# Kernel tuning notes

Measured on AMD Instinct MI355X. Metric: run time of the kernel, lower is better.

The kernel has to match this reference:

```python
import jax, jax.numpy as jnp
import numpy as np
import math

DIM = 1280
NUM_HEADS = 16
HEAD_DIM = DIM // NUM_HEADS  # 80
SEQ = 3072


def setup_inputs() -> dict:
    key = jax.random.key(0)
    ks = jax.random.split(key, 6)
    hidden_states = jax.random.normal(ks[0], (SEQ, DIM), dtype=jnp.float32)
    cu_seqlens = jnp.array([0, 768, 1536, 2304, 3072], dtype=jnp.int32)
    # rotary angles for half the head dim, as produced by the vision rotary embedding
    rotary_pos_emb = jax.random.uniform(ks[1], (SEQ, HEAD_DIM // 2), dtype=jnp.float32) * 10.0
    qkv_w = jax.random.normal(ks[2], (3 * DIM, DIM), dtype=jnp.float32) * (1.0 / math.sqrt(DIM))
    qkv_b = jax.random.normal(ks[3], (3 * DIM,), dtype=jnp.float32) * 0.02
    proj_w = jax.random.normal(ks[4], (DIM, DIM), dtype=jnp.float32) * (1.0 / math.sqrt(DIM))
    proj_b = jax.random.normal(ks[5], (DIM,), dtype=jnp.float32) * 0.02
    return {"hidden_states": hidden_states, "cu_seqlens": cu_seqlens,
            "rotary_pos_emb": rotary_pos_emb, "qkv_w": qkv_w, "qkv_b": qkv_b,
            "proj_w": proj_w, "proj_b": proj_b}


def _rotate_half(x):
    half = x.shape[-1] // 2
    return jnp.concatenate([-x[..., half:], x[..., :half]], axis=-1)


def _apply_rotary(t, rotary_pos_emb):
    # t: [seq, heads, head_dim]; rotary_pos_emb: [seq, head_dim//2]
    emb = jnp.concatenate([rotary_pos_emb, rotary_pos_emb], axis=-1)  # [seq, head_dim]
    cos = jnp.cos(emb)[:, None, :]
    sin = jnp.sin(emb)[:, None, :]
    return t * cos + _rotate_half(t) * sin


def reference(hidden_states, cu_seqlens, rotary_pos_emb, qkv_w, qkv_b, proj_w, proj_b):
    seq = hidden_states.shape[0]
    qkv = hidden_states @ qkv_w.T + qkv_b                       # [seq, 3*dim]
    qkv = qkv.reshape(seq, 3, NUM_HEADS, HEAD_DIM)
    q, k, v = qkv[:, 0], qkv[:, 1], qkv[:, 2]                   # [seq, h, d]
    q = _apply_rotary(q, rotary_pos_emb)
    k = _apply_rotary(k, rotary_pos_emb)

    # block-diagonal mask: token i attends to token j iff same segment
    seg = jnp.searchsorted(cu_seqlens[1:], jnp.arange(seq), side='right')
    same = seg[:, None] == seg[None, :]                         # [seq, seq] bool
    neg = jnp.finfo(q.dtype).min
    add_mask = jnp.where(same, jnp.float32(0), neg).astype(q.dtype)

    scale = 1.0 / math.sqrt(HEAD_DIM)
    scores = jnp.einsum('nhd,mhd->hnm', q, k) * scale           # [h, seq, seq]
    scores = scores + add_mask[None, :, :]
    attn = jax.nn.softmax(scores.astype(jnp.float32), axis=-1).astype(q.dtype)
    out = jnp.einsum('hnm,mhd->nhd', attn, v).reshape(seq, DIM)
    return out @ proj_w.T + proj_b
```

## Files before the change

### kernel.cpp

```cpp
#include <hip/hip_runtime.h>

#define SEQ 3072
#define NH 16
#define HD 80
#define SEGLEN 768

typedef unsigned short u16;
typedef unsigned int u32;
typedef float f32x4 __attribute__((ext_vector_type(4)));
typedef __bf16 bf16x8 __attribute__((ext_vector_type(8)));
typedef short short8 __attribute__((ext_vector_type(8)));
typedef u16 u16x4 __attribute__((ext_vector_type(4)));

#define WAITV(N) asm volatile("s_waitcnt vmcnt(" #N ")" ::: "memory")

__device__ __forceinline__ u16 f2bf(float f) {
  u32 u = __builtin_bit_cast(u32, f);
  u32 r = u + 0x7fffu + ((u >> 16) & 1u);
  return (u16)(r >> 16);
}
__device__ __forceinline__ float bf2f(u16 x) {
  u32 u = ((u32)x) << 16;
  return __builtin_bit_cast(float, u);
}

__device__ __forceinline__ f32x4 mfma16(short8 a, short8 b, f32x4 c) {
  return __builtin_amdgcn_mfma_f32_16x16x32_bf16(
      __builtin_bit_cast(bf16x8, a), __builtin_bit_cast(bf16x8, b), c, 0, 0, 0);
}

__device__ __forceinline__ void gload_lds16(const u16* g, u16* l) {
  __builtin_amdgcn_global_load_lds(
      (const __attribute__((address_space(1))) u32*)(g),
      (__attribute__((address_space(3))) u32*)(l), 16, 0, 0);
}

__global__ __launch_bounds__(256) void cvt3(const float* __restrict__ a, u16* __restrict__ ao, int na,
                                            const float* __restrict__ b, u16* __restrict__ bo, int nb,
                                            const float* __restrict__ c, u16* __restrict__ co, int nc) {
  int i = blockIdx.x * 256 + threadIdx.x;
  const float* src;
  u16* dst;
  int n;
  if (i < na) { src = a; dst = ao; n = i; }
  else if (i < na + nb) { src = b; dst = bo; n = i - na; }
  else if (i < na + nb + nc) { src = c; dst = co; n = i - na - nb; }
  else return;
  f32x4 v = ((const f32x4*)src)[n];
  u16x4 o;
  o[0] = f2bf(v[0]); o[1] = f2bf(v[1]); o[2] = f2bf(v[2]); o[3] = f2bf(v[3]);
  ((u16x4*)dst)[n] = o;
}

__global__ __launch_bounds__(512) void gemm_192(
    const u16* __restrict__ A, const u16* __restrict__ B,
    const float* __restrict__ bias, u16* __restrict__ C,
    int M, int N, int K) {
  __shared__ u16 LB[2 * 28672];
  char* lds = (char*)LB;
  const int tid = threadIdx.x, lane = tid & 63, w = tid >> 6;
  const int wm = w >> 2, wn = w & 3;
  const int lr = lane & 15, lg = lane >> 4;
  const int br = blockIdx.y * 192, bc = blockIdx.x * 256;
  const int NT = K >> 6;

  f32x4 acc[6][4];
#pragma unroll
  for (int m = 0; m < 6; ++m)
#pragma unroll
    for (int n = 0; n < 4; ++n) acc[m][n] = (f32x4){0.f, 0.f, 0.f, 0.f};

  const int chA0 = w * 96 + lane, chA1 = w * 96 + 64 + lane;
  const int chB0 = w * 128 + lane, chB1 = w * 128 + 64 + lane;
  auto srcptr = [&](const u16* Mx, int base, int ch, int Kd) {
    int row = ch >> 2, sl = ch & 3;
    return Mx + (size_t)(base + row) * Kd + (((sl - (row >> 1)) & 3) << 3);
  };
  const u16* sA0 = srcptr(A, br, chA0, K);
  const u16* sA1 = srcptr(A, br, chA1 < 768 ? chA1 : chA0, K);
  const u16* sB0 = srcptr(B, bc, chB0, K);
  const u16* sB1 = srcptr(B, bc, chB1, K);

  auto stgA = [&](int kcol, int buf, int half) {
    char* hb = lds + buf * 57344 + half * 12288;
    gload_lds16(sA0 + kcol, (u16*)(hb + chA0 * 16));
    if (lane < 32) gload_lds16(sA1 + kcol, (u16*)(hb + chA1 * 16));
  };
  auto stgB = [&](int kcol, int buf, int half) {
    char* hb = lds + buf * 57344 + 24576 + half * 16384;
    gload_lds16(sB0 + kcol, (u16*)(hb + chB0 * 16));
    gload_lds16(sB1 + kcol, (u16*)(hb + chB1 * 16));
  };

  int aoff[6], boff[4];
#pragma unroll
  for (int m = 0; m < 6; ++m) {
    int row = wm * 96 + m * 16 + lr;
    aoff[m] = row * 64 + ((lg + (row >> 1)) & 3) * 16;
  }
#pragma unroll
  for (int n = 0; n < 4; ++n) {
    int row = wn * 64 + n * 16 + lr;
    boff[n] = row * 64 + ((lg + (row >> 1)) & 3) * 16;
  }

  stgA(0, 0, 0); stgB(0, 0, 0);
  stgA(32, 0, 1); stgB(32, 0, 1);
  WAITV(4);
  __builtin_amdgcn_s_barrier();

  for (int t = 0; t < NT; ++t) {
    const int p = t & 1;
    const char* bufb = lds + p * 57344;
#pragma unroll
    for (int q = 0; q < 2; ++q) {
      const char* Ah = bufb + q * 12288;
      const char* Bh = bufb + 24576 + q * 16384;
      short8 af[6], bf[4];
#pragma unroll
      for (int m = 0; m < 6; ++m) af[m] = *(const short8*)(Ah + aoff[m]);
#pragma unroll
      for (int n = 0; n < 4; ++n) bf[n] = *(const short8*)(Bh + boff[n]);
      if (t + 1 < NT) {
        stgA((t + 1) * 64 + q * 32, p ^ 1, q);
        stgB((t + 1) * 64 + q * 32, p ^ 1, q);
      }
      __builtin_amdgcn_s_setprio(1);
#pragma unroll
      for (int m = 0; m < 6; ++m)
#pragma unroll
        for (int n = 0; n < 4; ++n) acc[m][n] = mfma16(af[m], bf[n], acc[m][n]);
      __builtin_amdgcn_s_setprio(0);
      if (t + 1 < NT) {
        WAITV(4);
        __builtin_amdgcn_s_barrier();
      } else if (q == 0) {
        WAITV(0);
        __builtin_amdgcn_s_barrier();
      }
    }
  }

#pragma unroll
  for (int n = 0; n < 4; ++n) {
    int col = bc + wn * 64 + n * 16 + lr;
    float bv = bias[col];
#pragma unroll
    for (int m = 0; m < 6; ++m) {
      int rowb = br + wm * 96 + m * 16 + lg * 4;
#pragma unroll
      for (int r = 0; r < 4; ++r)
        C[(size_t)(rowb + r) * N + col] = f2bf(acc[m][n][r] + bv);
    }
  }
}

template <int OUT_BF16, int WM, int WN>
__global__ __launch_bounds__(256) void gemm_p3(
    const u16* __restrict__ A, const u16* __restrict__ B,
    const float* __restrict__ bias, void* __restrict__ Cv,
    int M, int N, int K) {
  constexpr int BM = 32 * WM, BN = 32 * WN;
  constexpr int ROWS = BM + BN;
  constexpr int L = ROWS / 64;
  static_assert(L == 3, "tuned for L=3");
  __shared__ u16 LB[3][ROWS * 32];
  const int tid = threadIdx.x, lane = tid & 63, w = tid >> 6;
  const int wr = (w >> 1) * (WM * 16), wc = (w & 1) * (WN * 16);
  const int lr = lane & 15, lg = lane >> 4;
  const int gy = gridDim.y;
  const int fc = blockIdx.x * gy + blockIdx.y;
  const int cpx = (gridDim.x * gy) >> 3;
  const int f = (fc & 7) * cpx + (fc >> 3);
  const int bx = f / gy, by = f % gy;
  const int br = by * BM, bc = bx * BN;
  const int NT = K >> 5;

  f32x4 acc[WM][WN];
#pragma unroll
  for (int m = 0; m < WM; ++m)
#pragma unroll
    for (int n = 0; n < WN; ++n) acc[m][n] = (f32x4){0.f, 0.f, 0.f, 0.f};

  const u16* sp[L];
#pragma unroll
  for (int c = 0; c < L; ++c) {
    int ch = c * 256 + tid;
    int row = ch >> 2, sl = ch & 3;
    int scol = ((sl - (row >> 1)) & 3) << 3;
    sp[c] = (row < BM ? A + (br + row) * (size_t)K
                      : B + (bc + row - BM) * (size_t)K) + scol;
  }
  auto stage = [&](int t, int buf) {
#pragma unroll
    for (int c = 0; c < L; ++c)
      gload_lds16(sp[c] + t * 32, &LB[buf][(c * 256 + tid) * 8]);
  };

  int aoff[WM], boff[WN];
#pragma unroll
  for (int m = 0; m < WM; ++m) {
    int row = wr + m * 16 + lr;
    aoff[m] = row * 64 + ((lg + (row >> 1)) & 3) * 16;
  }
#pragma unroll
  for (int n = 0; n < WN; ++n) {
    int row = BM + wc + n * 16 + lr;
    boff[n] = row * 64 + ((lg + (row >> 1)) & 3) * 16;
  }

  auto step = [&](int t, int buf, bool issue, int wn) {
    if (issue) stage(t + 2, (t + 2) % 3);
    const char* base = (const char*)&LB[buf][0];
    short8 af[WM], bf[WN];
#pragma unroll
    for (int m = 0; m < WM; ++m) af[m] = *(const short8*)(base + aoff[m]);
#pragma unroll
    for (int n = 0; n < WN; ++n) bf[n] = *(const short8*)(base + boff[n]);
#pragma unroll
    for (int m = 0; m < WM; ++m)
#pragma unroll
      for (int n = 0; n < WN; ++n) acc[m][n] = mfma16(af[m], bf[n], acc[m][n]);
    if (wn == 3) WAITV(3);
    else if (wn == 0) WAITV(0);
    if (wn >= 0) __builtin_amdgcn_s_barrier();
  };

  stage(0, 0);
  stage(1, 1);
  WAITV(3);
  __builtin_amdgcn_s_barrier();

  int t = 0;
  for (; t + 3 <= NT - 2; t += 3) {
    step(t + 0, 0, true, 3);
    step(t + 1, 1, true, 3);
    step(t + 2, 2, true, 3);
  }
  step(NT - 4, 0, true, 3);
  step(NT - 3, 1, true, 3);
  step(NT - 2, 2, false, 0);
  step(NT - 1, 0, false, -1);

#pragma unroll
  for (int n = 0; n < WN; ++n) {
    int col = bc + wc + n * 16 + lr;
    float bv = bias[col];
#pragma unroll
    for (int m = 0; m < WM; ++m) {
      int rowb = br + wr + m * 16 + lg * 4;
#pragma unroll
      for (int r = 0; r < 4; ++r) {
        float v = acc[m][n][r] + bv;
        if (OUT_BF16)
          ((u16*)Cv)[(rowb + r) * N + col] = f2bf(v);
        else
          ((float*)Cv)[(rowb + r) * N + col] = v;
      }
    }
  }
}

__global__ __launch_bounds__(256) void prep_kern(
    const u16* __restrict__ qkvb, const float* __restrict__ rpe,
    u16* __restrict__ qb, u16* __restrict__ kb, u16* __restrict__ vt) {
  const int bid = blockIdx.x, tid = threadIdx.x;
  if (bid < 3072) {
    const float QSCL = 0.16129841769519493f;
    const u16* row = qkvb + bid * 3840;
#pragma unroll
    for (int it = 0; it < 5; ++it) {
      int idx = it * 256 + tid;
      int d = idx % 80;
      float e = rpe[bid * 40 + (d % 40)];
      float s, c;
      sincosf(e, &s, &c);
      float qv = bf2f(row[idx]);
      float qo = (d < 40) ? -bf2f(row[idx + 40]) : bf2f(row[idx - 40]);
      float kv = bf2f(row[1280 + idx]);
      float ko = (d < 40) ? -bf2f(row[1280 + idx + 40]) : bf2f(row[1280 + idx - 40]);
      int o = bid * 1280 + idx;
      qb[o] = f2bf((qv * c + qo * s) * QSCL);
      kb[o] = f2bf(kv * c + ko * s);
    }
  } else {
    __shared__ u16 tile[64 * 84];
    const int vb = bid - 3072;
    const int s0 = (vb % 48) * 64, h = vb / 48;
#pragma unroll
    for (int c = 0; c < 20; ++c) {
      int ch = c * 256 + tid;
      int r = ch / 80, d = ch % 80;
      tile[r * 84 + d] = qkvb[(s0 + r) * 3840 + 2560 + h * 80 + d];
    }
    __syncthreads();
#pragma unroll
    for (int c = 0; c < 20; ++c) {
      int ch = c * 256 + tid;
      int d = ch >> 6, r = ch & 63;
      vt[(h * 96 + d) * 3072 + s0 + r] = tile[r * 84 + d];
    }
    if (tid < 64) vt[(h * 96 + 80) * 3072 + s0 + tid] = 0x3F80;
  }
}

__global__ __launch_bounds__(256) void attn_kern(
    const u16* __restrict__ qb, const u16* __restrict__ kb,
    const u16* __restrict__ vt, u16* __restrict__ ob) {
  __shared__ u16 SH[26176];
  char* shb = (char*)SH;
  const int tid = threadIdx.x, lane = tid & 63, w = tid >> 6;
  const int lr = lane & 15, lg = lane >> 4;
  const int xcd = blockIdx.x & 7, t = blockIdx.x >> 3;
  const int qt = t % 12, shhi = t / 12;
  const int sh = xcd + shhi * 8;
  const int seg = sh >> 4, h = sh & 15;
  const int qrow = seg * SEGLEN + qt * 64 + w * 16 + lr;

  short8 qf[3];
#pragma unroll
  for (int kk = 0; kk < 3; ++kk) {
    int d = kk * 32 + lg * 8;
    if (d < 80)
      qf[kk] = *(const short8*)(qb + qrow * 1280 + h * 80 + d);
    else
      qf[kk] = (short8){0, 0, 0, 0, 0, 0, 0, 0};
  }
  f32x4 oa[6];
#pragma unroll
  for (int n = 0; n < 6; ++n) oa[n] = (f32x4){0.f, 0.f, 0.f, 0.f};
  float mrow[4] = {-1e30f, -1e30f, -1e30f, -1e30f};

  const u16* kseg = kb + seg * SEGLEN * 1280 + h * 80;
  const u16* vseg = vt + (h * 96) * 3072 + seg * SEGLEN;

  auto stageK = [&](int buf, int it) {
    const u16* kbase = kseg + it * 64 * 1280;
#pragma unroll
    for (int c = 0; c < 4; ++c) {
      int ch = c * 256 + tid;
      int kv = ch >> 4, sl = ch & 15;
      gload_lds16(kbase + kv * 1280 + ((sl ^ (kv & 7)) << 3),
                  (u16*)(shb + buf * 16384 + ch * 16));
    }
  };
  auto stageV = [&](int it) {
    const u16* vbase = vseg + it * 64;
#pragma unroll
    for (int c = 0; c < 3; ++c) {
      int ch = c * 256 + tid;
      if (ch < 648) {
        int d = ch >> 3, sl = ch & 7;
        gload_lds16(vbase + d * 3072 + ((sl ^ (d & 7)) << 3),
                    (u16*)(shb + 32768 + ch * 16));
      }
    }
  };

  stageK(0, 0);
  stageV(0);
  __syncthreads();
  int cur = 0;
  char* PsW = shb + 43136 + w * 2304;
  const char* Vc = shb + 32768;

  for (int it = 0; it < 12; ++it) {
    if (it > 0) stageV(it);
    if (it < 11) stageK(cur ^ 1, it + 1);
    const char* Kc = shb + cur * 16384;
    f32x4 sf[4];
#pragma unroll
    for (int n = 0; n < 4; ++n) {
      sf[n] = (f32x4){0.f, 0.f, 0.f, 0.f};
#pragma unroll
      for (int kk = 0; kk < 3; ++kk) {
        int row = n * 16 + lr;
        int X = kk * 64 + lg * 16;
        short8 kf = *(const short8*)(Kc + row * 256 + (X ^ ((row & 7) << 4)));
        __builtin_amdgcn_s_setprio(1);
        sf[n] = mfma16(qf[kk], kf, sf[n]);
        __builtin_amdgcn_s_setprio(0);
      }
    }
    float mx[4];
#pragma unroll
    for (int r = 0; r < 4; ++r) {
      float a = fmaxf(fmaxf(sf[0][r], sf[1][r]), fmaxf(sf[2][r], sf[3][r]));
      a = fmaxf(a, __shfl_xor(a, 1, 16));
      a = fmaxf(a, __shfl_xor(a, 2, 16));
      a = fmaxf(a, __shfl_xor(a, 4, 16));
      a = fmaxf(a, __shfl_xor(a, 8, 16));
      mx[r] = a;
    }
    float need = fmaxf(fmaxf(mx[0] - mrow[0], mx[1] - mrow[1]),
                       fmaxf(mx[2] - mrow[2], mx[3] - mrow[3]));
    if (!__all(need <= 8.0f)) {
#pragma unroll
      for (int r = 0; r < 4; ++r) {
        float m = fmaxf(mrow[r], mx[r]);
        float f = exp2f(mrow[r] - m);
        mrow[r] = m;
#pragma unroll
        for (int n = 0; n < 6; ++n) oa[n][r] *= f;
      }
    }
#pragma unroll
    for (int r = 0; r < 4; ++r) {
      float p0 = exp2f(sf[0][r] - mrow[r]), p1 = exp2f(sf[1][r] - mrow[r]);
      float p2 = exp2f(sf[2][r] - mrow[r]), p3 = exp2f(sf[3][r] - mrow[r]);
      int offb = (lg * 4 + r) * 144 + lr * 2;
      *(u16*)(PsW + offb + ((lg ^ 0) << 5)) = f2bf(p0);
      *(u16*)(PsW + offb + ((lg ^ 1) << 5)) = f2bf(p1);
      *(u16*)(PsW + offb + ((lg ^ 2) << 5)) = f2bf(p2);
      *(u16*)(PsW + offb + ((lg ^ 3) << 5)) = f2bf(p3);
    }
    __syncthreads();
#pragma unroll
    for (int kt = 0; kt < 2; ++kt) {
      short8 pf = *(const short8*)(PsW + lr * 144 +
                                   ((((kt << 1) + (lg >> 1)) ^ (lr >> 2)) << 5) +
                                   ((lg & 1) << 4));
#pragma unroll
      for (int n = 0; n < 6; ++n) {
        int dcol = n * 16 + lr;
        int X = kt * 64 + lg * 16;
        short8 vf = *(const short8*)(Vc + dcol * 128 + (X ^ ((dcol & 7) << 4)));
        __builtin_amdgcn_s_setprio(1);
        oa[n] = mfma16(pf, vf, oa[n]);
        __builtin_amdgcn_s_setprio(0);
      }
    }
    __syncthreads();
    cur ^= 1;
  }
#pragma unroll
  for (int r = 0; r < 4; ++r) {
    float lsum = __shfl(oa[5][r], lane & 48, 64);
    float linv = 1.0f / lsum;
    int orow = seg * SEGLEN + qt * 64 + w * 16 + lg * 4 + r;
#pragma unroll
    for (int n = 0; n < 5; ++n)
      ob[orow * 1280 + h * 80 + n * 16 + lr] = f2bf(oa[n][r] * linv);
  }
}

extern "C" void kernel_launch(void* const* d_in, const int* in_sizes, int n_in,
                              void* d_out, int out_size, void* d_ws, size_t ws_size,
                              hipStream_t stream) {
  const float* hs = (const float*)d_in[0];
  const float* rpe = (const float*)d_in[2];
  const float* qkvw = (const float*)d_in[3];
  const float* qkv_b = (const float*)d_in[4];
  const float* pw = (const float*)d_in[5];
  const float* pb = (const float*)d_in[6];
  float* out = (float*)d_out;

  char* ws = (char*)d_ws;
  u16* hsb = (u16*)(ws);
  u16* wqkvb = (u16*)(ws + 7864320);
  u16* wprojb = (u16*)(ws + 17694720);
  u16* qkvb = (u16*)(ws + 20971520);
  u16* vt = (u16*)(ws + 44564480);
  u16* qb = hsb;
  u16* kb = wqkvb;
  u16* aob = qkvb;

  cvt3<<<10240, 256, 0, stream>>>(hs, hsb, 983040, qkvw, wqkvb, 1228800, pw, wprojb, 409600);
  gemm_192<<<dim3(15, 16), 512, 0, stream>>>(hsb, wqkvb, qkv_b, qkvb, 3072, 3840, 1280);
  prep_kern<<<3840, 256, 0, stream>>>(qkvb, rpe, qb, kb, vt);
  attn_kern<<<768, 256, 0, stream>>>(qb, kb, vt, aob);
  gemm_p3<0, 2, 4><<<dim3(10, 48), 256, 0, stream>>>(aob, wprojb, pb, out, 3072, 1280, 1280);
}
```

Measured before the change: 127.0 us.

## Process two query sub-tiles per wave in attention with half the threads

The attention kernel now runs 128 threads per block, and each wave handles 32 query rows as two 16-row MFMA tiles. Each K and V fragment read from LDS is reused for two MFMAs. The aim is to cut LDS read traffic and block-level overhead per query row. In exchange, register pressure roughly doubles for accumulators and Q fragments, each thread issues twice as many staging loads, and fewer waves are available to hide latency.

After: 136.2 us. 1.07x slower.

```diff
diff --git a/kernel.cpp b/kernel.cpp
--- a/kernel.cpp
+++ b/kernel.cpp
@@ -304,7 +304,7 @@
   }
 }
 
-__global__ __launch_bounds__(256) void attn_kern(
+__global__ __launch_bounds__(128) void attn_kern(
     const u16* __restrict__ qb, const u16* __restrict__ kb,
     const u16* __restrict__ vt, u16* __restrict__ ob) {
   __shared__ u16 SH[26176];
@@ -315,21 +315,26 @@
   const int qt = t % 12, shhi = t / 12;
   const int sh = xcd + shhi * 8;
   const int seg = sh >> 4, h = sh & 15;
-  const int qrow = seg * SEGLEN + qt * 64 + w * 16 + lr;
-
-  short8 qf[3];
-#pragma unroll
-  for (int kk = 0; kk < 3; ++kk) {
-    int d = kk * 32 + lg * 8;
-    if (d < 80)
-      qf[kk] = *(const short8*)(qb + qrow * 1280 + h * 80 + d);
-    else
-      qf[kk] = (short8){0, 0, 0, 0, 0, 0, 0, 0};
-  }
-  f32x4 oa[6];
-#pragma unroll
-  for (int n = 0; n < 6; ++n) oa[n] = (f32x4){0.f, 0.f, 0.f, 0.f};
-  float mrow[4] = {-1e30f, -1e30f, -1e30f, -1e30f};
+  const int qbase = seg * SEGLEN + qt * 64 + w * 32;
+
+  short8 qf[2][3];
+#pragma unroll
+  for (int m = 0; m < 2; ++m)
+#pragma unroll
+    for (int kk = 0; kk < 3; ++kk) {
+      int d = kk * 32 + lg * 8;
+      if (d < 80)
+        qf[m][kk] = *(const short8*)(qb + (qbase + m * 16 + lr) * 1280 + h * 80 + d);
+      else
+        qf[m][kk] = (short8){0, 0, 0, 0, 0, 0, 0, 0};
+    }
+  f32x4 oa[2][6];
+#pragma unroll
+  for (int m = 0; m < 2; ++m)
+#pragma unroll
+    for (int n = 0; n < 6; ++n) oa[m][n] = (f32x4){0.f, 0.f, 0.f, 0.f};
+  float mrow[2][4] = {{-1e30f, -1e30f, -1e30f, -1e30f},
+                      {-1e30f, -1e30f, -1e30f, -1e30f}};
 
   const u16* kseg = kb + seg * SEGLEN * 1280 + h * 80;
   const u16* vseg = vt + (h * 96) * 3072 + seg * SEGLEN;
@@ -337,8 +342,8 @@
   auto stageK = [&](int buf, int it) {
     const u16* kbase = kseg + it * 64 * 1280;
 #pragma unroll
-    for (int c = 0; c < 4; ++c) {
-      int ch = c * 256 + tid;
+    for (int c = 0; c < 8; ++c) {
+      int ch = c * 128 + tid;
       int kv = ch >> 4, sl = ch & 15;
       gload_lds16(kbase + kv * 1280 + ((sl ^ (kv & 7)) << 3),
                   (u16*)(shb + buf * 16384 + ch * 16));
@@ -347,8 +352,8 @@
   auto stageV = [&](int it) {
     const u16* vbase = vseg + it * 64;
 #pragma unroll
-    for (int c = 0; c < 3; ++c) {
-      int ch = c * 256 + tid;
+    for (int c = 0; c < 6; ++c) {
+      int ch = c * 128 + tid;
       if (ch < 648) {
         int d = ch >> 3, sl = ch & 7;
         gload_lds16(vbase + d * 3072 + ((sl ^ (d & 7)) << 3),
@@ -361,72 +366,80 @@
   stageV(0);
   __syncthreads();
   int cur = 0;
-  char* PsW = shb + 43136 + w * 2304;
+  char* PsW[2] = {shb + 43136 + (w * 2 + 0) * 2304, shb + 43136 + (w * 2 + 1) * 2304};
   const char* Vc = shb + 32768;
 
   for (int it = 0; it < 12; ++it) {
     if (it > 0) stageV(it);
     if (it < 11) stageK(cur ^ 1, it + 1);
     const char* Kc = shb + cur * 16384;
-    f32x4 sf[4];
+    f32x4 sf[2][4];
+#pragma unroll
+    for (int m = 0; m < 2; ++m)
+#pragma unroll
+      for (int n = 0; n < 4; ++n) sf[m][n] = (f32x4){0.f, 0.f, 0.f, 0.f};
 #pragma unroll
     for (int n = 0; n < 4; ++n) {
-      sf[n] = (f32x4){0.f, 0.f, 0.f, 0.f};
 #pragma unroll
       for (int kk = 0; kk < 3; ++kk) {
         int row = n * 16 + lr;
         int X = kk * 64 + lg * 16;
         short8 kf = *(const short8*)(Kc + row * 256 + (X ^ ((row & 7) << 4)));
         __builtin_amdgcn_s_setprio(1);
-        sf[n] = mfma16(qf[kk], kf, sf[n]);
+        sf[0][n] = mfma16(qf[0][kk], kf, sf[0][n]);
+        sf[1][n] = mfma16(qf[1][kk], kf, sf[1][n]);
         __builtin_amdgcn_s_setprio(0);
       }
     }
-    float mx[4];
-#pragma unroll
-    for (int r = 0; r < 4; ++r) {
-      float a = fmaxf(fmaxf(sf[0][r], sf[1][r]), fmaxf(sf[2][r], sf[3][r]));
-      a = fmaxf(a, __shfl_xor(a, 1, 16));
-      a = fmaxf(a, __shfl_xor(a, 2, 16));
-      a = fmaxf(a, __shfl_xor(a, 4, 16));
-      a = fmaxf(a, __shfl_xor(a, 8, 16));
-      mx[r] = a;
-    }
-    float need = fmaxf(fmaxf(mx[0] - mrow[0], mx[1] - mrow[1]),
-                       fmaxf(mx[2] - mrow[2], mx[3] - mrow[3]));
-    if (!__all(need <= 8.0f)) {
+#pragma unroll
+    for (int m = 0; m < 2; ++m) {
+      float mx[4];
 #pragma unroll
       for (int r = 0; r < 4; ++r) {
-        float m = fmaxf(mrow[r], mx[r]);
-        float f = exp2f(mrow[r] - m);
-        mrow[r] = m;
-#pragma unroll
-        for (int n = 0; n < 6; ++n) oa[n][r] *= f;
-      }
-    }
-#pragma unroll
-    for (int r = 0; r < 4; ++r) {
-      float p0 = exp2f(sf[0][r] - mrow[r]), p1 = exp2f(sf[1][r] - mrow[r]);
-      float p2 = exp2f(sf[2][r] - mrow[r]), p3 = exp2f(sf[3][r] - mrow[r]);
-      int offb = (lg * 4 + r) * 144 + lr * 2;
-      *(u16*)(PsW + offb + ((lg ^ 0) << 5)) = f2bf(p0);
-      *(u16*)(PsW + offb + ((lg ^ 1) << 5)) = f2bf(p1);
-      *(u16*)(PsW + offb + ((lg ^ 2) << 5)) = f2bf(p2);
-      *(u16*)(PsW + offb + ((lg ^ 3) << 5)) = f2bf(p3);
+        float a = fmaxf(fmaxf(sf[m][0][r], sf[m][1][r]), fmaxf(sf[m][2][r], sf[m][3][r]));
+        a = fmaxf(a, __shfl_xor(a, 1, 16));
+        a = fmaxf(a, __shfl_xor(a, 2, 16));
+        a = fmaxf(a, __shfl_xor(a, 4, 16));
+        a = fmaxf(a, __shfl_xor(a, 8, 16));
+        mx[r] = a;
+      }
+      float need = fmaxf(fmaxf(mx[0] - mrow[m][0], mx[1] - mrow[m][1]),
+                         fmaxf(mx[2] - mrow[m][2], mx[3] - mrow[m][3]));
+      if (!__all(need <= 8.0f)) {
+#pragma unroll
+        for (int r = 0; r < 4; ++r) {
+          float mm = fmaxf(mrow[m][r], mx[r]);
+          float f = exp2f(mrow[m][r] - mm);
+          mrow[m][r] = mm;
+#pragma unroll
+          for (int n = 0; n < 6; ++n) oa[m][n][r] *= f;
+        }
+      }
+#pragma unroll
+      for (int r = 0; r < 4; ++r) {
+        float p0 = exp2f(sf[m][0][r] - mrow[m][r]), p1 = exp2f(sf[m][1][r] - mrow[m][r]);
+        float p2 = exp2f(sf[m][2][r] - mrow[m][r]), p3 = exp2f(sf[m][3][r] - mrow[m][r]);
+        int offb = (lg * 4 + r) * 144 + lr * 2;
+        *(u16*)(PsW[m] + offb + ((lg ^ 0) << 5)) = f2bf(p0);
+        *(u16*)(PsW[m] + offb + ((lg ^ 1) << 5)) = f2bf(p1);
+        *(u16*)(PsW[m] + offb + ((lg ^ 2) << 5)) = f2bf(p2);
+        *(u16*)(PsW[m] + offb + ((lg ^ 3) << 5)) = f2bf(p3);
+      }
     }
     __syncthreads();
 #pragma unroll
     for (int kt = 0; kt < 2; ++kt) {
-      short8 pf = *(const short8*)(PsW + lr * 144 +
-                                   ((((kt << 1) + (lg >> 1)) ^ (lr >> 2)) << 5) +
-                                   ((lg & 1) << 4));
+      const int pswz = lr * 144 + ((((kt << 1) + (lg >> 1)) ^ (lr >> 2)) << 5) + ((lg & 1) << 4);
+      short8 pf0 = *(const short8*)(PsW[0] + pswz);
+      short8 pf1 = *(const short8*)(PsW[1] + pswz);
 #pragma unroll
       for (int n = 0; n < 6; ++n) {
         int dcol = n * 16 + lr;
         int X = kt * 64 + lg * 16;
         short8 vf = *(const short8*)(Vc + dcol * 128 + (X ^ ((dcol & 7) << 4)));
         __builtin_amdgcn_s_setprio(1);
-        oa[n] = mfma16(pf, vf, oa[n]);
+        oa[0][n] = mfma16(pf0, vf, oa[0][n]);
+        oa[1][n] = mfma16(pf1, vf, oa[1][n]);
         __builtin_amdgcn_s_setprio(0);
       }
     }
@@ -434,14 +447,16 @@
     cur ^= 1;
   }
 #pragma unroll
-  for (int r = 0; r < 4; ++r) {
-    float lsum = __shfl(oa[5][r], lane & 48, 64);
-    float linv = 1.0f / lsum;
-    int orow = seg * SEGLEN + qt * 64 + w * 16 + lg * 4 + r;
-#pragma unroll
-    for (int n = 0; n < 5; ++n)
-      ob[orow * 1280 + h * 80 + n * 16 + lr] = f2bf(oa[n][r] * linv);
-  }
+  for (int m = 0; m < 2; ++m)
+#pragma unroll
+    for (int r = 0; r < 4; ++r) {
+      float lsum = __shfl(oa[m][5][r], lane & 48, 64);
+      float linv = 1.0f / lsum;
+      int orow = qbase + m * 16 + lg * 4 + r;
+#pragma unroll
+      for (int n = 0; n < 5; ++n)
+        ob[orow * 1280 + h * 80 + n * 16 + lr] = f2bf(oa[m][n][r] * linv);
+    }
 }
 
 extern "C" void kernel_launch(void* const* d_in, const int* in_sizes, int n_in,
@@ -468,6 +483,6 @@
   cvt3<<<10240, 256, 0, stream>>>(hs, hsb, 983040, qkvw, wqkvb, 1228800, pw, wprojb, 409600);
   gemm_192<<<dim3(15, 16), 512, 0, stream>>>(hsb, wqkvb, qkv_b, qkvb, 3072, 3840, 1280);
   prep_kern<<<3840, 256, 0, stream>>>(qkvb, rpe, qb, kb, vt);
-  attn_kern<<<768, 256, 0, stream>>>(qb, kb, vt, aob);
+  attn_kern<<<768, 128, 0, stream>>>(qb, kb, vt, aob);
   gemm_p3<0, 2, 4><<<dim3(10, 48), 256, 0, stream>>>(aob, wprojb, pb, out, 3072, 1280, 1280);
 }
```

## Fuse rotary embedding and V transpose into QKV GEMM epilogue

Applied to the files above, without the earlier changes.

Removes the separate prep kernel. The QKV GEMM now stages its output tile in LDS and writes rotary-applied, scaled Q and K, plus a transposed V, directly to their buffers. The QKV weight rows for Q and K are permuted during fp32-to-bf16 conversion so rotary pairs (d, d+40) sit in adjacent columns. The conversion kernel also writes the ones-row of V^T. This saves one launch and a round trip of the intermediate qkv buffer, at the cost of a heavier GEMM epilogue with strided V^T stores.

After: 123.5 us. 1.03x faster.

```diff
diff --git a/kernel.cpp b/kernel.cpp
--- a/kernel.cpp
+++ b/kernel.cpp
@@ -35,27 +35,46 @@
       (__attribute__((address_space(3))) u32*)(l), 16, 0, 0);
 }
 
-__global__ __launch_bounds__(256) void cvt3(const float* __restrict__ a, u16* __restrict__ ao, int na,
-                                            const float* __restrict__ b, u16* __restrict__ bo, int nb,
-                                            const float* __restrict__ c, u16* __restrict__ co, int nc) {
+__global__ __launch_bounds__(256) void cvt3p(
+    const float* __restrict__ a, u16* __restrict__ ao, int na,
+    const float* __restrict__ b, u16* __restrict__ bo, int nb,
+    const float* __restrict__ c, u16* __restrict__ co, int nc,
+    u16* __restrict__ vt) {
   int i = blockIdx.x * 256 + threadIdx.x;
-  const float* src;
-  u16* dst;
-  int n;
-  if (i < na) { src = a; dst = ao; n = i; }
-  else if (i < na + nb) { src = b; dst = bo; n = i - na; }
-  else if (i < na + nb + nc) { src = c; dst = co; n = i - na - nb; }
-  else return;
-  f32x4 v = ((const f32x4*)src)[n];
-  u16x4 o;
-  o[0] = f2bf(v[0]); o[1] = f2bf(v[1]); o[2] = f2bf(v[2]); o[3] = f2bf(v[3]);
-  ((u16x4*)dst)[n] = o;
+  if (i < na) {
+    f32x4 v = ((const f32x4*)a)[i];
+    u16x4 o = {f2bf(v[0]), f2bf(v[1]), f2bf(v[2]), f2bf(v[3])};
+    ((u16x4*)ao)[i] = o;
+  } else if (i < na + nb) {
+    int n = i - na;
+    int row = n / 320, col4 = n % 320;
+    int dstrow = row;
+    if (row < 2560) {
+      int sec = row / 1280, rr = row - sec * 1280;
+      int h = rr / 80, dd = rr % 80;
+      dstrow = sec * 1280 + h * 80 + 2 * (dd % 40) + (dd >= 40 ? 1 : 0);
+    }
+    f32x4 v = ((const f32x4*)b)[n];
+    u16x4 o = {f2bf(v[0]), f2bf(v[1]), f2bf(v[2]), f2bf(v[3])};
+    ((u16x4*)bo)[dstrow * 320 + col4] = o;
+  } else if (i < na + nb + nc) {
+    int n = i - na - nb;
+    f32x4 v = ((const f32x4*)c)[n];
+    u16x4 o = {f2bf(v[0]), f2bf(v[1]), f2bf(v[2]), f2bf(v[3])};
+    ((u16x4*)co)[n] = o;
+  } else if (i < na + nb + nc + 12288) {
+    int j = i - na - nb - nc;
+    int h = j / 768, s4 = (j % 768) * 4;
+    u16x4 o = {0x3F80, 0x3F80, 0x3F80, 0x3F80};
+    *(u16x4*)(vt + (size_t)(h * 96 + 80) * 3072 + s4) = o;
+  }
 }
 
 __global__ __launch_bounds__(512) void gemm_192(
     const u16* __restrict__ A, const u16* __restrict__ B,
-    const float* __restrict__ bias, u16* __restrict__ C,
-    int M, int N, int K) {
+    const float* __restrict__ bias, const float* __restrict__ rpe,
+    u16* __restrict__ qbg, u16* __restrict__ kbg, u16* __restrict__ vtg,
+    int K) {
   __shared__ u16 LB[2 * 28672];
   char* lds = (char*)LB;
   const int tid = threadIdx.x, lane = tid & 63, w = tid >> 6;
@@ -72,14 +91,14 @@
 
   const int chA0 = w * 96 + lane, chA1 = w * 96 + 64 + lane;
   const int chB0 = w * 128 + lane, chB1 = w * 128 + 64 + lane;
-  auto srcptr = [&](const u16* Mx, int base, int ch, int Kd) {
+  auto srcptr = [&](const u16* Mx, int base, int ch) {
     int row = ch >> 2, sl = ch & 3;
-    return Mx + (size_t)(base + row) * Kd + (((sl - (row >> 1)) & 3) << 3);
-  };
-  const u16* sA0 = srcptr(A, br, chA0, K);
-  const u16* sA1 = srcptr(A, br, chA1 < 768 ? chA1 : chA0, K);
-  const u16* sB0 = srcptr(B, bc, chB0, K);
-  const u16* sB1 = srcptr(B, bc, chB1, K);
+    return Mx + (size_t)(base + row) * K + (((sl - (row >> 1)) & 3) << 3);
+  };
+  const u16* sA0 = srcptr(A, br, chA0);
+  const u16* sA1 = srcptr(A, br, chA1 < 768 ? chA1 : chA0);
+  const u16* sB0 = srcptr(B, bc, chB0);
+  const u16* sB1 = srcptr(B, bc, chB1);
 
   auto stgA = [&](int kcol, int buf, int half) {
     char* hb = lds + buf * 57344 + half * 12288;
@@ -141,16 +160,58 @@
     }
   }
 
-#pragma unroll
-  for (int n = 0; n < 4; ++n) {
-    int col = bc + wn * 64 + n * 16 + lr;
-    float bv = bias[col];
-#pragma unroll
-    for (int m = 0; m < 6; ++m) {
-      int rowb = br + wm * 96 + m * 16 + lg * 4;
-#pragma unroll
-      for (int r = 0; r < 4; ++r)
-        C[(size_t)(rowb + r) * N + col] = f2bf(acc[m][n][r] + bv);
+  const int sec = blockIdx.x / 5;
+  __syncthreads();
+  {
+    float bv[4];
+#pragma unroll
+    for (int n = 0; n < 4; ++n) {
+      int col_l = wn * 64 + n * 16 + lr;
+      int gc = (bc - sec * 1280) + col_l;
+      int h = gc / 80, cc = gc % 80;
+      int d = (sec < 2) ? ((cc >> 1) + ((cc & 1) ? 40 : 0)) : cc;
+      bv[n] = bias[sec * 1280 + h * 80 + d];
+    }
+#pragma unroll
+    for (int n = 0; n < 4; ++n) {
+      int col_l = wn * 64 + n * 16 + lr;
+#pragma unroll
+      for (int m = 0; m < 6; ++m) {
+        int rowb = wm * 96 + m * 16 + lg * 4;
+#pragma unroll
+        for (int r = 0; r < 4; ++r)
+          *(u16*)(lds + (size_t)(rowb + r) * 514 + col_l * 2) = f2bf(acc[m][n][r] + bv[n]);
+      }
+    }
+  }
+  __syncthreads();
+  if (sec == 2) {
+#pragma unroll
+    for (int e = 0; e < 96; ++e) {
+      int idx = e * 512 + tid;
+      int col = idx / 192, row = idx % 192;
+      u16 val = *(const u16*)(lds + (size_t)row * 514 + col * 2);
+      int gc = bc - 2560 + col;
+      int h = gc / 80, d = gc % 80;
+      vtg[(size_t)(h * 96 + d) * 3072 + br + row] = val;
+    }
+  } else {
+    u16* outb = sec ? kbg : qbg;
+    const float scale = sec ? 1.0f : 0.16129841769519493f;
+#pragma unroll
+    for (int e = 0; e < 48; ++e) {
+      int idx = e * 512 + tid;
+      int row = idx >> 7, cp = idx & 127;
+      float v0 = bf2f(*(const u16*)(lds + (size_t)row * 514 + cp * 4));
+      float v1 = bf2f(*(const u16*)(lds + (size_t)row * 514 + cp * 4 + 2));
+      int gc = bc - sec * 1280 + cp * 2;
+      int h = gc / 80, dpair = (gc % 80) >> 1;
+      float ang = rpe[(br + row) * 40 + dpair];
+      float s, c;
+      sincosf(ang, &s, &c);
+      size_t ob_ = (size_t)(br + row) * 1280 + h * 80 + dpair;
+      outb[ob_] = f2bf((v0 * c - v1 * s) * scale);
+      outb[ob_ + 40] = f2bf((v1 * c + v0 * s) * scale);
     }
   }
 }
@@ -261,49 +322,6 @@
   }
 }
 
-__global__ __launch_bounds__(256) void prep_kern(
-    const u16* __restrict__ qkvb, const float* __restrict__ rpe,
-    u16* __restrict__ qb, u16* __restrict__ kb, u16* __restrict__ vt) {
-  const int bid = blockIdx.x, tid = threadIdx.x;
-  if (bid < 3072) {
-    const float QSCL = 0.16129841769519493f;
-    const u16* row = qkvb + bid * 3840;
-#pragma unroll
-    for (int it = 0; it < 5; ++it) {
-      int idx = it * 256 + tid;
-      int d = idx % 80;
-      float e = rpe[bid * 40 + (d % 40)];
-      float s, c;
-      sincosf(e, &s, &c);
-      float qv = bf2f(row[idx]);
-      float qo = (d < 40) ? -bf2f(row[idx + 40]) : bf2f(row[idx - 40]);
-      float kv = bf2f(row[1280 + idx]);
-      float ko = (d < 40) ? -bf2f(row[1280 + idx + 40]) : bf2f(row[1280 + idx - 40]);
-      int o = bid * 1280 + idx;
-      qb[o] = f2bf((qv * c + qo * s) * QSCL);
-      kb[o] = f2bf(kv * c + ko * s);
-    }
-  } else {
-    __shared__ u16 tile[64 * 84];
-    const int vb = bid - 3072;
-    const int s0 = (vb % 48) * 64, h = vb / 48;
-#pragma unroll
-    for (int c = 0; c < 20; ++c) {
-      int ch = c * 256 + tid;
-      int r = ch / 80, d = ch % 80;
-      tile[r * 84 + d] = qkvb[(s0 + r) * 3840 + 2560 + h * 80 + d];
-    }
-    __syncthreads();
-#pragma unroll
-    for (int c = 0; c < 20; ++c) {
-      int ch = c * 256 + tid;
-      int d = ch >> 6, r = ch & 63;
-      vt[(h * 96 + d) * 3072 + s0 + r] = tile[r * 84 + d];
-    }
-    if (tid < 64) vt[(h * 96 + 80) * 3072 + s0 + tid] = 0x3F80;
-  }
-}
-
 __global__ __launch_bounds__(256) void attn_kern(
     const u16* __restrict__ qb, const u16* __restrict__ kb,
     const u16* __restrict__ vt, u16* __restrict__ ob) {
@@ -459,15 +477,14 @@
   u16* hsb = (u16*)(ws);
   u16* wqkvb = (u16*)(ws + 7864320);
   u16* wprojb = (u16*)(ws + 17694720);
-  u16* qkvb = (u16*)(ws + 20971520);
-  u16* vt = (u16*)(ws + 44564480);
-  u16* qb = hsb;
-  u16* kb = wqkvb;
-  u16* aob = qkvb;
-
-  cvt3<<<10240, 256, 0, stream>>>(hs, hsb, 983040, qkvw, wqkvb, 1228800, pw, wprojb, 409600);
-  gemm_192<<<dim3(15, 16), 512, 0, stream>>>(hsb, wqkvb, qkv_b, qkvb, 3072, 3840, 1280);
-  prep_kern<<<3840, 256, 0, stream>>>(qkvb, rpe, qb, kb, vt);
+  u16* qb = (u16*)(ws + 20971520);
+  u16* kb = (u16*)(ws + 28835840);
+  u16* vt = (u16*)(ws + 36700160);
+  u16* aob = (u16*)(ws + 46137344);
+
+  cvt3p<<<10288, 256, 0, stream>>>(hs, hsb, 983040, qkvw, wqkvb, 1228800,
+                                   pw, wprojb, 409600, vt);
+  gemm_192<<<dim3(15, 16), 512, 0, stream>>>(hsb, wqkvb, qkv_b, rpe, qb, kb, vt, 1280);
   attn_kern<<<768, 256, 0, stream>>>(qb, kb, vt, aob);
   gemm_p3<0, 2, 4><<<dim3(10, 48), 256, 0, stream>>>(aob, wprojb, pb, out, 3072, 1280, 1280);
 }
```
